# Performance work log

Measured on AMD Instinct MI355X. Metric: run time of the kernel, lower is better.

The kernel has to match this reference:

```python
import jax, jax.numpy as jnp
import numpy as np

KS = 3  # kernel_size
PAD = 1  # padding


def setup_inputs() -> dict:
    key = jax.random.key(0)
    ks = jax.random.split(key, 5)
    b, c, h, w = 8, 64, 512, 512
    x = jax.random.normal(ks[0], (b, c, h, w), dtype=jnp.float32)
    w1 = jax.random.normal(ks[1], (c, c), dtype=jnp.float32) * 0.05
    b1 = jax.random.normal(ks[2], (c,), dtype=jnp.float32) * 0.05
    w2 = jax.random.normal(ks[3], (KS * KS, c), dtype=jnp.float32) * 0.05
    b2 = jax.random.normal(ks[4], (KS * KS,), dtype=jnp.float32) * 0.05
    return {"x": x, "w1": w1, "b1": b1, "w2": w2, "b2": b2}


def reference(x, w1, b1, w2, b2):
    b, c, h, w = x.shape
    # SEKG: global average pool -> 1x1 conv -> LeakyReLU(0.2) -> 1x1 conv
    feat = x.mean(axis=(2, 3))                      # [b, c]
    h1 = feat @ w1.T + b1                           # [b, c]
    h1 = jnp.where(h1 > 0, h1, 0.2 * h1)            # LeakyReLU(0.2)
    k = h1 @ w2.T + b2                              # [b, KS*KS]
    k = k.reshape(b, KS, KS)
    k = k / (k.sum(axis=(1, 2), keepdims=True) + 1e-6)  # normalize per-sample kernel
    # per-sample depthwise conv: fold batch into groups
    kern = jnp.broadcast_to(k[:, None], (b, c, KS, KS)).reshape(b * c, 1, KS, KS)
    xr = x.reshape(1, b * c, h, w)
    out = jax.lax.conv_general_dilated(
        xr, kern,
        window_strides=(1, 1),
        padding=[(PAD, PAD), (PAD, PAD)],
        feature_group_count=b * c,
        dimension_numbers=("NCHW", "OIHW", "NCHW"),
    )
    return out.reshape(b, c, h, w)
```

## Files before the change

kernel.cpp:

```cpp
#include <hip/hip_runtime.h>

#define HH 512
#define WW 512
#define HW (HH * WW)

typedef float f32x4 __attribute__((ext_vector_type(4)));

__global__ __launch_bounds__(256) void pool_kernel(const float* __restrict__ x,
                                                   float* __restrict__ partial) {
    const int blk = blockIdx.x;
    const int plane = blk >> 2;
    const int strip = blk & 3;
    const float4* p = reinterpret_cast<const float4*>(x + (size_t)plane * HW) +
                      (size_t)strip * (HW / 16);
    float s = 0.f;
    #pragma unroll 4
    for (int i = threadIdx.x; i < HW / 16; i += 256) {
        float4 v = p[i];
        s += (v.x + v.y) + (v.z + v.w);
    }
    #pragma unroll
    for (int off = 32; off > 0; off >>= 1) s += __shfl_down(s, off, 64);
    __shared__ float wsum[4];
    const int lane = threadIdx.x & 63;
    const int wid  = threadIdx.x >> 6;
    if (lane == 0) wsum[wid] = s;
    __syncthreads();
    if (threadIdx.x == 0) partial[blk] = (wsum[0] + wsum[1]) + (wsum[2] + wsum[3]);
}

__global__ __launch_bounds__(512) void make_kernels(const float* __restrict__ partial,
                                                    const float* __restrict__ w1,
                                                    const float* __restrict__ b1,
                                                    const float* __restrict__ w2,
                                                    const float* __restrict__ b2,
                                                    float* __restrict__ kout) {
    __shared__ float feat[512];
    __shared__ float h1[512];
    __shared__ float kr[72];
    __shared__ float ksum[8];
    const int t = threadIdx.x;
    feat[t] = (partial[4*t] + partial[4*t+1] + partial[4*t+2] + partial[4*t+3]) *
              (1.0f / (float)HW);
    __syncthreads();
    const int b = t >> 6, j = t & 63;
    float s = b1[j];
    const float* wr = w1 + j * 64;
    const float* fb = feat + b * 64;
    #pragma unroll 8
    for (int c = 0; c < 64; ++c) s += fb[c] * wr[c];
    h1[t] = (s > 0.f) ? s : 0.2f * s;
    __syncthreads();
    if (t < 72) {
        const int bb = t / 9, q = t - bb * 9;
        float s2 = b2[q];
        const float* hb = h1 + bb * 64;
        const float* wq = w2 + q * 64;
        #pragma unroll 8
        for (int c = 0; c < 64; ++c) s2 += hb[c] * wq[c];
        kr[t] = s2;
    }
    __syncthreads();
    if (t < 8) {
        float s3 = 0.f;
        #pragma unroll
        for (int q = 0; q < 9; ++q) s3 += kr[t * 9 + q];
        ksum[t] = s3 + 1e-6f;
    }
    __syncthreads();
    if (t < 72) kout[t] = kr[t] / ksum[t / 9];
}

__device__ __forceinline__ void load_row6(float r[6], const float* __restrict__ plane,
                                          int y, int x0) {
    if ((unsigned)y >= (unsigned)HH) {
        r[0] = r[1] = r[2] = r[3] = r[4] = r[5] = 0.f;
        return;
    }
    const float* row = plane + (size_t)y * WW;
    r[0] = (x0 > 0) ? row[x0 - 1] : 0.f;
    const float4 m = *reinterpret_cast<const float4*>(row + x0);
    r[1] = m.x; r[2] = m.y; r[3] = m.z; r[4] = m.w;
    r[5] = (x0 + 4 < WW) ? row[x0 + 4] : 0.f;
}

__global__ __launch_bounds__(256) void conv_kernel(const float* __restrict__ x,
                                                   const float* __restrict__ kall,
                                                   float* __restrict__ out) {
    const int gid    = blockIdx.x * 256 + threadIdx.x;
    const int xseg   = gid & 127;
    const int ystrip = (gid >> 7) & 31;
    const int plane  = gid >> 12;
    const int b      = plane >> 6;
    float k[9];
    #pragma unroll
    for (int i = 0; i < 9; ++i) k[i] = kall[b * 9 + i];
    const float* xp = x + (size_t)plane * HW;
    float* op       = out + (size_t)plane * HW;
    const int x0 = xseg * 4;
    const int y0 = ystrip * 16;

    float r0[6], r1[6], r2[6];
    load_row6(r0, xp, y0 - 1, x0);
    load_row6(r1, xp, y0,     x0);
    #pragma unroll
    for (int i = 0; i < 16; ++i) {
        load_row6(r2, xp, y0 + i + 1, x0);
        f32x4 o;
        #pragma unroll
        for (int j = 0; j < 4; ++j) {
            o[j] = k[0]*r0[j] + k[1]*r0[j+1] + k[2]*r0[j+2]
                 + k[3]*r1[j] + k[4]*r1[j+1] + k[5]*r1[j+2]
                 + k[6]*r2[j] + k[7]*r2[j+1] + k[8]*r2[j+2];
        }
        __builtin_nontemporal_store(o,
            reinterpret_cast<f32x4*>(op + (size_t)(y0 + i) * WW + x0));
        #pragma unroll
        for (int q = 0; q < 6; ++q) { r0[q] = r1[q]; r1[q] = r2[q]; }
    }
}

extern "C" void kernel_launch(void* const* d_in, const int* in_sizes, int n_in,
                              void* d_out, int out_size, void* d_ws, size_t ws_size,
                              hipStream_t stream) {
    const float* x  = (const float*)d_in[0];
    const float* w1 = (const float*)d_in[1];
    const float* b1 = (const float*)d_in[2];
    const float* w2 = (const float*)d_in[3];
    const float* b2 = (const float*)d_in[4];
    float* out = (float*)d_out;

    float* partial = (float*)d_ws;
    float* kout    = partial + 2048;

    pool_kernel<<<2048, 256, 0, stream>>>(x, partial);
    make_kernels<<<1, 512, 0, stream>>>(partial, w1, b1, w2, b2, kout);
    conv_kernel<<<8192, 256, 0, stream>>>(x, kout, out);
}
```

Baseline: 294.4 us.

## Pipeline pooling and convolution across batches in fused staged launches

Replaces the separate pool, kernel-generation and conv launches with nine launches of one staged kernel. Each launch convolves batch i-1, computing that batch's 3x3 kernel inside every conv block, while other blocks pool batch i. The aim is for batch i-1's conv read of x to still find the data in cache after batch i-1 was pooled one launch earlier, and to overlap pooling with conv. In exchange it adds launch overhead, every conv block redundantly recomputes the small MLP, and the per-launch grids are smaller.

```diff
diff --git a/kernel.cpp b/kernel.cpp
--- a/kernel.cpp
+++ b/kernel.cpp
@@ -5,71 +5,6 @@
 #define HW (HH * WW)
 
 typedef float f32x4 __attribute__((ext_vector_type(4)));
-
-__global__ __launch_bounds__(256) void pool_kernel(const float* __restrict__ x,
-                                                   float* __restrict__ partial) {
-    const int blk = blockIdx.x;
-    const int plane = blk >> 2;
-    const int strip = blk & 3;
-    const float4* p = reinterpret_cast<const float4*>(x + (size_t)plane * HW) +
-                      (size_t)strip * (HW / 16);
-    float s = 0.f;
-    #pragma unroll 4
-    for (int i = threadIdx.x; i < HW / 16; i += 256) {
-        float4 v = p[i];
-        s += (v.x + v.y) + (v.z + v.w);
-    }
-    #pragma unroll
-    for (int off = 32; off > 0; off >>= 1) s += __shfl_down(s, off, 64);
-    __shared__ float wsum[4];
-    const int lane = threadIdx.x & 63;
-    const int wid  = threadIdx.x >> 6;
-    if (lane == 0) wsum[wid] = s;
-    __syncthreads();
-    if (threadIdx.x == 0) partial[blk] = (wsum[0] + wsum[1]) + (wsum[2] + wsum[3]);
-}
-
-__global__ __launch_bounds__(512) void make_kernels(const float* __restrict__ partial,
-                                                    const float* __restrict__ w1,
-                                                    const float* __restrict__ b1,
-                                                    const float* __restrict__ w2,
-                                                    const float* __restrict__ b2,
-                                                    float* __restrict__ kout) {
-    __shared__ float feat[512];
-    __shared__ float h1[512];
-    __shared__ float kr[72];
-    __shared__ float ksum[8];
-    const int t = threadIdx.x;
-    feat[t] = (partial[4*t] + partial[4*t+1] + partial[4*t+2] + partial[4*t+3]) *
-              (1.0f / (float)HW);
-    __syncthreads();
-    const int b = t >> 6, j = t & 63;
-    float s = b1[j];
-    const float* wr = w1 + j * 64;
-    const float* fb = feat + b * 64;
-    #pragma unroll 8
-    for (int c = 0; c < 64; ++c) s += fb[c] * wr[c];
-    h1[t] = (s > 0.f) ? s : 0.2f * s;
-    __syncthreads();
-    if (t < 72) {
-        const int bb = t / 9, q = t - bb * 9;
-        float s2 = b2[q];
-        const float* hb = h1 + bb * 64;
-        const float* wq = w2 + q * 64;
-        #pragma unroll 8
-        for (int c = 0; c < 64; ++c) s2 += hb[c] * wq[c];
-        kr[t] = s2;
-    }
-    __syncthreads();
-    if (t < 8) {
-        float s3 = 0.f;
-        #pragma unroll
-        for (int q = 0; q < 9; ++q) s3 += kr[t * 9 + q];
-        ksum[t] = s3 + 1e-6f;
-    }
-    __syncthreads();
-    if (t < 72) kout[t] = kr[t] / ksum[t / 9];
-}
 
 __device__ __forceinline__ void load_row6(float r[6], const float* __restrict__ plane,
                                           int y, int x0) {
@@ -84,39 +19,104 @@
     r[5] = (x0 + 4 < WW) ? row[x0 + 4] : 0.f;
 }
 
-__global__ __launch_bounds__(256) void conv_kernel(const float* __restrict__ x,
-                                                   const float* __restrict__ kall,
-                                                   float* __restrict__ out) {
-    const int gid    = blockIdx.x * 256 + threadIdx.x;
-    const int xseg   = gid & 127;
-    const int ystrip = (gid >> 7) & 31;
-    const int plane  = gid >> 12;
-    const int b      = plane >> 6;
-    float k[9];
-    #pragma unroll
-    for (int i = 0; i < 9; ++i) k[i] = kall[b * 9 + i];
-    const float* xp = x + (size_t)plane * HW;
-    float* op       = out + (size_t)plane * HW;
-    const int x0 = xseg * 4;
-    const int y0 = ystrip * 16;
+__global__ __launch_bounds__(256) void stage_kernel(
+        const float* __restrict__ x, float* __restrict__ out,
+        float* __restrict__ partial,
+        const float* __restrict__ w1, const float* __restrict__ b1,
+        const float* __restrict__ w2, const float* __restrict__ b2,
+        int ib, int nconv) {
+    const int blk = blockIdx.x;
+    const int t = threadIdx.x;
 
-    float r0[6], r1[6], r2[6];
-    load_row6(r0, xp, y0 - 1, x0);
-    load_row6(r1, xp, y0,     x0);
-    #pragma unroll
-    for (int i = 0; i < 16; ++i) {
-        load_row6(r2, xp, y0 + i + 1, x0);
-        f32x4 o;
+    if (blk < nconv) {
+        const int b = ib - 1;
+        __shared__ float feat[64];
+        __shared__ float h1s[64];
+        __shared__ float kks[10];
+        if (t < 64) {
+            const float* p4 = partial + (size_t)(b * 64 + t) * 4;
+            feat[t] = (p4[0] + p4[1] + p4[2] + p4[3]) * (1.0f / (float)HW);
+        }
+        __syncthreads();
+        if (t < 64) {
+            float s = b1[t];
+            const float* wr = w1 + t * 64;
+            #pragma unroll 8
+            for (int c = 0; c < 64; ++c) s += feat[c] * wr[c];
+            h1s[t] = (s > 0.f) ? s : 0.2f * s;
+        }
+        __syncthreads();
+        if (t < 9) {
+            float s2 = b2[t];
+            const float* wq = w2 + t * 64;
+            #pragma unroll 8
+            for (int c = 0; c < 64; ++c) s2 += h1s[c] * wq[c];
+            kks[t] = s2;
+        }
+        __syncthreads();
+        if (t == 0) {
+            float s3 = 0.f;
+            #pragma unroll
+            for (int q = 0; q < 9; ++q) s3 += kks[q];
+            kks[9] = s3 + 1e-6f;
+        }
+        __syncthreads();
+        float k[9];
+        {
+            const float ks = kks[9];
+            #pragma unroll
+            for (int q = 0; q < 9; ++q) k[q] = kks[q] / ks;
+        }
+
+        const int plane_local = blk >> 4;
+        const int plane = b * 64 + plane_local;
+        const int xseg = t & 127;
+        const int ystrip = ((blk & 15) << 1) | (t >> 7);
+        const float* xp = x + (size_t)plane * HW;
+        float* op       = out + (size_t)plane * HW;
+        const int x0 = xseg * 4;
+        const int y0 = ystrip * 16;
+
+        float r0[6], r1[6], r2[6];
+        load_row6(r0, xp, y0 - 1, x0);
+        load_row6(r1, xp, y0,     x0);
         #pragma unroll
-        for (int j = 0; j < 4; ++j) {
-            o[j] = k[0]*r0[j] + k[1]*r0[j+1] + k[2]*r0[j+2]
-                 + k[3]*r1[j] + k[4]*r1[j+1] + k[5]*r1[j+2]
-                 + k[6]*r2[j] + k[7]*r2[j+1] + k[8]*r2[j+2];
+        for (int i = 0; i < 16; ++i) {
+            load_row6(r2, xp, y0 + i + 1, x0);
+            f32x4 o;
+            #pragma unroll
+            for (int j = 0; j < 4; ++j) {
+                o[j] = k[0]*r0[j] + k[1]*r0[j+1] + k[2]*r0[j+2]
+                     + k[3]*r1[j] + k[4]*r1[j+1] + k[5]*r1[j+2]
+                     + k[6]*r2[j] + k[7]*r2[j+1] + k[8]*r2[j+2];
+            }
+            __builtin_nontemporal_store(o,
+                reinterpret_cast<f32x4*>(op + (size_t)(y0 + i) * WW + x0));
+            #pragma unroll
+            for (int q = 0; q < 6; ++q) { r0[q] = r1[q]; r1[q] = r2[q]; }
         }
-        __builtin_nontemporal_store(o,
-            reinterpret_cast<f32x4*>(op + (size_t)(y0 + i) * WW + x0));
+    } else {
+        const int pblk = blk - nconv;
+        const int plane = ib * 64 + (pblk >> 2);
+        const int strip = pblk & 3;
+        const float4* p = reinterpret_cast<const float4*>(x + (size_t)plane * HW) +
+                          (size_t)strip * (HW / 16);
+        float s = 0.f;
+        #pragma unroll 4
+        for (int i = t; i < HW / 16; i += 256) {
+            float4 v = p[i];
+            s += (v.x + v.y) + (v.z + v.w);
+        }
         #pragma unroll
-        for (int q = 0; q < 6; ++q) { r0[q] = r1[q]; r1[q] = r2[q]; }
+        for (int off = 32; off > 0; off >>= 1) s += __shfl_down(s, off, 64);
+        __shared__ float wsum[4];
+        const int lane = t & 63;
+        const int wid  = t >> 6;
+        if (lane == 0) wsum[wid] = s;
+        __syncthreads();
+        if (t == 0)
+            partial[(size_t)plane * 4 + strip] =
+                (wsum[0] + wsum[1]) + (wsum[2] + wsum[3]);
     }
 }
 
@@ -129,11 +129,10 @@
     const float* w2 = (const float*)d_in[3];
     const float* b2 = (const float*)d_in[4];
     float* out = (float*)d_out;
+    float* partial = (float*)d_ws;
 
-    float* partial = (float*)d_ws;
-    float* kout    = partial + 2048;
-
-    pool_kernel<<<2048, 256, 0, stream>>>(x, partial);
-    make_kernels<<<1, 512, 0, stream>>>(partial, w1, b1, w2, b2, kout);
-    conv_kernel<<<8192, 256, 0, stream>>>(x, kout, out);
+    stage_kernel<<<256, 256, 0, stream>>>(x, out, partial, w1, b1, w2, b2, 0, 0);
+    for (int i = 1; i <= 7; ++i)
+        stage_kernel<<<1280, 256, 0, stream>>>(x, out, partial, w1, b1, w2, b2, i, 1024);
+    stage_kernel<<<1024, 256, 0, stream>>>(x, out, partial, w1, b1, w2, b2, 8, 1024);
 }
```

Result: slower. 302.2 us (+2.6%).
